# Kernel tuning notes

Measured on AMD Instinct MI355X. Metric: run time of the kernel, lower is better.

Reference implementation:

```python
import jax, jax.numpy as jnp
import numpy as np

NB, HD, NL, NF = 5, 64, 4, 10           # num_bins, hidden_dim(d_model), num_layers, num_frames
DI, DS, DC, DTR = 128, 16, 4, 4          # d_inner=2*HD, d_state, d_conv, dt_rank=ceil(HD/16)
B, H, W = 4, 64, 64


def _conv2d(x, w, b):
    y = jax.lax.conv_general_dilated(x, w, (1, 1), 'SAME',
                                     dimension_numbers=('NCHW', 'OIHW', 'NCHW'))
    return y + b[None, :, None, None]


def _bn_relu(x, gamma, beta, eps=1e-5):
    # BatchNorm2d in training mode: biased batch stats over (N,H,W)
    mean = x.mean(axis=(0, 2, 3), keepdims=True)
    var = x.var(axis=(0, 2, 3), keepdims=True)
    y = (x - mean) * jax.lax.rsqrt(var + eps)
    return jax.nn.relu(y * gamma[None, :, None, None] + beta[None, :, None, None])


def _silu(x):
    return x * jax.nn.sigmoid(x)


def _causal_dwconv(x, w, b):
    # x: (B,L,DI), w: (DI,K) depthwise causal conv, b: (DI,)
    K = w.shape[1]
    L = x.shape[1]
    xp = jnp.pad(x, ((0, 0), (K - 1, 0), (0, 0)))
    y = sum(xp[:, k:k + L, :] * w[:, k] for k in range(K))
    return y + b


def _selective_scan(u, delta, A, Bm, Cm, D):
    # u,delta: (B,L,DI); A: (DI,DS); Bm,Cm: (B,L,DS); D: (DI,)
    dT, BT, CT, uT = (t.transpose(1, 0, 2) for t in (delta, Bm, Cm, u))
    h0 = jnp.zeros((u.shape[0], A.shape[0], A.shape[1]), u.dtype)

    def step(h, inp):
        d_t, B_t, C_t, u_t = inp                     # (B,DI),(B,DS),(B,DS),(B,DI)
        dA = jnp.exp(d_t[:, :, None] * A)            # (B,DI,DS)
        h = dA * h + (d_t * u_t)[:, :, None] * B_t[:, None, :]
        y = jnp.einsum('bds,bs->bd', h, C_t)
        return h, y

    _, ys = jax.lax.scan(step, h0, (dT, BT, CT, uT))  # ys: (L,B,DI)
    return ys.transpose(1, 0, 2) + u * D


def _mamba(x, in_proj, conv_w, conv_b, x_proj, dt_w, dt_b, A_log, Dp, out_proj):
    xz = x @ in_proj.T                               # (B,L,2*DI)
    xi, z = jnp.split(xz, 2, axis=-1)
    xi = _silu(_causal_dwconv(xi, conv_w, conv_b))
    xdbc = xi @ x_proj.T                             # (B,L,DTR+2*DS)
    dt, Bm, Cm = jnp.split(xdbc, [DTR, DTR + DS], axis=-1)
    delta = jax.nn.softplus(dt @ dt_w.T + dt_b)
    A = -jnp.exp(A_log)
    y = _selective_scan(xi, delta, A, Bm, Cm, Dp)
    return (y * _silu(z)) @ out_proj.T


def setup_inputs() -> dict:
    key = jax.random.key(0)
    ks = jax.random.split(key, 20)
    s = 0.02
    inp = {
        'x': jax.random.normal(ks[0], (B, NB, H, W), jnp.float32),
        'enc_w': jax.random.normal(ks[1], (HD, NB, 3, 3), jnp.float32) * s,
        'enc_b': jnp.zeros((HD,), jnp.float32),
        'enc_g': jnp.ones((HD,), jnp.float32),
        'enc_be': jnp.zeros((HD,), jnp.float32),
        'in_proj': jax.random.normal(ks[2], (NL, 2 * DI, HD), jnp.float32) * s,
        'conv_w': jax.random.normal(ks[3], (NL, DI, DC), jnp.float32) * s,
        'conv_b': jnp.zeros((NL, DI), jnp.float32),
        'x_proj': jax.random.normal(ks[4], (NL, DTR + 2 * DS, DI), jnp.float32) * s,
        'dt_w': jax.random.normal(ks[5], (NL, DI, DTR), jnp.float32) * s,
        'dt_b': jax.random.normal(ks[6], (NL, DI), jnp.float32) * 0.1 - 4.0,
        'A_log': jnp.broadcast_to(jnp.log(jnp.arange(1, DS + 1, dtype=jnp.float32)),
                                  (NL, DI, DS)).copy(),
        'Dp': jnp.ones((NL, DI), jnp.float32),
        'out_proj': jax.random.normal(ks[7], (NL, HD, DI), jnp.float32) * s,
        'dec1_w': jax.random.normal(ks[8], (HD, HD, 3, 3), jnp.float32) * s,
        'dec1_b': jnp.zeros((HD,), jnp.float32),
        'dec1_g': jnp.ones((HD,), jnp.float32),
        'dec1_be': jnp.zeros((HD,), jnp.float32),
        'dec2_w': jax.random.normal(ks[9], (NF, HD, 3, 3), jnp.float32) * s,
        'dec2_b': jnp.zeros((NF,), jnp.float32),
    }
    return inp


def reference(x, enc_w, enc_b, enc_g, enc_be, in_proj, conv_w, conv_b, x_proj,
              dt_w, dt_b, A_log, Dp, out_proj, dec1_w, dec1_b, dec1_g, dec1_be,
              dec2_w, dec2_b):
    Bb, _, Hh, Ww = x.shape
    h = _bn_relu(_conv2d(x, enc_w, enc_b), enc_g, enc_be)   # (B,HD,H,W)
    t = h.reshape(Bb, HD, Hh * Ww).transpose(0, 2, 1)        # (B,L,HD)
    for i in range(NL):
        t = t + _mamba(t, in_proj[i], conv_w[i], conv_b[i], x_proj[i],
                       dt_w[i], dt_b[i], A_log[i], Dp[i], out_proj[i])
    h = t.transpose(0, 2, 1).reshape(Bb, HD, Hh, Ww)
    h = _bn_relu(_conv2d(h, dec1_w, dec1_b), dec1_g, dec1_be)
    return _conv2d(h, dec2_w, dec2_b)                        # (B,NF,H,W)
```

## Files before the change

### kernel.cpp

```cpp
#include <hip/hip_runtime.h>
#include <hip/hip_bf16.h>

#define BB   4
#define NBC  5
#define HD   64
#define NLAYER 4
#define NFC  10
#define DIM  128
#define DSN  16
#define DCN  4
#define DTRK 4
#define HH   64
#define WWD  64
#define LL   4096
#define MM   (BB*LL)
#define CLEN   32
#define NCHUNK 128

#define A4GET(a, i) (((i) & 3) == 0 ? (a)[(i) >> 2].x : ((i) & 3) == 1 ? (a)[(i) >> 2].y : \
                     ((i) & 3) == 2 ? (a)[(i) >> 2].z : (a)[(i) >> 2].w)

__global__ void k_prep_all(const float* __restrict__ in_proj, const float* __restrict__ out_proj,
                           const float* __restrict__ dec1_w, const float* __restrict__ dec2_w,
                           float* __restrict__ wTin, float* __restrict__ wTout,
                           float* __restrict__ wT1, float* __restrict__ wT2,
                           float* __restrict__ stats, float* __restrict__ stats2) {
    int idx = blockIdx.x * blockDim.x + threadIdx.x;
    if (idx < 65536) {
        int n = idx & 255, k = (idx >> 8) & 63, l = idx >> 14;
        wTin[idx] = in_proj[(l << 14) + (n << 6) + k];
    } else if (idx < 98304) {
        int j = idx - 65536;
        int n = j & 63, k = (j >> 6) & 127, l = j >> 13;
        wTout[j] = out_proj[(l << 13) + (n << 7) + k];
    } else if (idx < 135168) {
        int j = idx - 98304;
        int co = j & 63, tap = (j >> 6) % 9, ci = j / 576;
        wT1[j] = dec1_w[co * 576 + ci * 9 + tap];
    } else if (idx < 142848) {
        int j = idx - 135168;
        int tap = j % 12, t2 = j / 12, co = t2 % NFC, ci = t2 / NFC;
        wT2[j] = (tap < 9) ? dec2_w[co * 576 + ci * 9 + tap] : 0.f;
    } else if (idx < 143104) {
        int j = idx - 142848;
        if (j < 128) stats[j] = 0.f; else stats2[j - 128] = 0.f;
    }
}

__global__ void k_enc_conv(const float* __restrict__ x, const float* __restrict__ w,
                           const float* __restrict__ bias, float* __restrict__ out,
                           float* __restrict__ stats) {
    __shared__ float r1[256], r2[256];
    int tid = threadIdx.x;
    int idx = blockIdx.x * 256 + tid;
    int wx = idx & 63;
    int hy = (idx >> 6) & 63;
    int co = (idx >> 12) & 63;
    int b  = idx >> 18;
    float acc = bias[co];
    for (int ci = 0; ci < NBC; ++ci) {
        const float* xin = x + (((long)(b * NBC + ci)) << 12);
        const float* wp  = w + (co * NBC + ci) * 9;
        #pragma unroll
        for (int kh = 0; kh < 3; ++kh) {
            int ih = hy + kh - 1;
            if (ih < 0 || ih >= HH) continue;
            #pragma unroll
            for (int kw = 0; kw < 3; ++kw) {
                int iw = wx + kw - 1;
                if (iw < 0 || iw >= WWD) continue;
                acc += xin[(ih << 6) + iw] * wp[kh * 3 + kw];
            }
        }
    }
    out[idx] = acc;
    r1[tid] = acc; r2[tid] = acc * acc;
    __syncthreads();
    for (int off = 128; off > 0; off >>= 1) {
        if (tid < off) { r1[tid] += r1[tid + off]; r2[tid] += r2[tid + off]; }
        __syncthreads();
    }
    if (tid == 0) {
        atomicAdd(&stats[co], r1[0]);
        atomicAdd(&stats[64 + co], r2[0]);
    }
}

__global__ __launch_bounds__(256, 1) void k_gemm_in_bn(const float* __restrict__ src,
                                                       const float* __restrict__ stats,
                                                       const float* __restrict__ g,
                                                       const float* __restrict__ be,
                                                       const float* __restrict__ wT,
                                                       float* __restrict__ tout,
                                                       float* __restrict__ xz) {
    __shared__ __align__(16) float ts[64 * 68];
    __shared__ float sc[64], sh[64];
    long m0 = (long)blockIdx.x << 6;
    int b = (int)(m0 >> 12);
    int hw0 = (int)(m0 & 4095);
    int tid = threadIdx.x;
    if (tid < 64) {
        float m = stats[tid] * (1.f / 16384.f);
        float var = stats[64 + tid] * (1.f / 16384.f) - m * m;
        float ss = g[tid] * rsqrtf(var + 1e-5f);
        sc[tid] = ss; sh[tid] = be[tid] - m * ss;
    }
    __syncthreads();
    for (int i = tid; i < 4096; i += 256) {
        int pix = i & 63, c = i >> 6;
        float v = src[(((long)((b << 6) + c)) << 12) + hw0 + pix];
        ts[pix * 68 + c] = fmaxf(v * sc[c] + sh[c], 0.f);
    }
    __syncthreads();
    for (int i = tid; i < 4096; i += 256) {
        int r = i >> 6, c = i & 63;
        tout[(m0 + r) * 64 + c] = ts[r * 68 + c];
    }
    int rg = tid >> 5;
    int cg = tid & 31;
    float acc[8][8] = {};
    int n0 = cg << 3;
    for (int k4 = 0; k4 < 16; ++k4) {
        float4 a[8];
        #pragma unroll
        for (int r2 = 0; r2 < 8; ++r2)
            a[r2] = *(const float4*)&ts[((rg << 3) + r2) * 68 + (k4 << 2)];
        #pragma unroll
        for (int kk = 0; kk < 4; ++kk) {
            const float* wr = wT + (((k4 << 2) + kk) << 8) + n0;
            float4 w0 = *(const float4*)&wr[0];
            float4 w1 = *(const float4*)&wr[4];
            #pragma unroll
            for (int r2 = 0; r2 < 8; ++r2) {
                float av = (kk == 0) ? a[r2].x : (kk == 1) ? a[r2].y
                         : (kk == 2) ? a[r2].z : a[r2].w;
                acc[r2][0] += av * w0.x; acc[r2][1] += av * w0.y;
                acc[r2][2] += av * w0.z; acc[r2][3] += av * w0.w;
                acc[r2][4] += av * w1.x; acc[r2][5] += av * w1.y;
                acc[r2][6] += av * w1.z; acc[r2][7] += av * w1.w;
            }
        }
    }
    #pragma unroll
    for (int r2 = 0; r2 < 8; ++r2) {
        long m = m0 + (rg << 3) + r2;
        *(float4*)&xz[(m << 8) + n0]     = make_float4(acc[r2][0], acc[r2][1], acc[r2][2], acc[r2][3]);
        *(float4*)&xz[(m << 8) + n0 + 4] = make_float4(acc[r2][4], acc[r2][5], acc[r2][6], acc[r2][7]);
    }
}

__global__ __launch_bounds__(512, 4) void k_xproj_fused(
        const float* __restrict__ xz, const float* __restrict__ cw,
        const float* __restrict__ cb, const float* __restrict__ Wx,
        const float* __restrict__ dw, const float* __restrict__ dbias,
        const float* __restrict__ A_log,
        float* __restrict__ xiT, float* __restrict__ deltaT,
        float* __restrict__ xdbc, float* __restrict__ Pb, float* __restrict__ Sb) {
    __shared__ __align__(16) float xz_s[35 * 132];
    __shared__ __align__(16) float xi_s[32 * 132];
    __shared__ __align__(16) float w_s[36 * 132];
    __shared__ __align__(16) float xs[32 * 40];
    __shared__ float cwT[4 * 128];
    __shared__ float cb_s[128];
    long m0 = (long)blockIdx.x << 5;
    int l0 = (int)(m0 & 4095);
    int tid = threadIdx.x;

    for (int i = tid; i < 35 * 32; i += 512) {
        int j = i >> 5, c4 = (i & 31) << 2;
        float4 v = make_float4(0.f, 0.f, 0.f, 0.f);
        if (l0 - 3 + j >= 0) v = *(const float4*)&xz[(m0 - 3 + j) * 256 + c4];
        *(float4*)&xz_s[j * 132 + c4] = v;
    }
    if (tid < 128) cb_s[tid] = cb[tid];
    { int kk = tid >> 7, dii = tid & 127; if (tid < 512) cwT[(kk << 7) + dii] = cw[(dii << 2) + kk]; }
    for (int i = tid; i < 1152; i += 512) {
        int n = i >> 5, c4 = (i & 31) << 2;
        *(float4*)&w_s[n * 132 + c4] = *(const float4*)&Wx[(n << 7) + c4];
    }
    __syncthreads();

    #pragma unroll
    for (int ii = 0; ii < 2; ++ii) {
        int i = tid + (ii << 9);
        int r = i >> 5, d4 = (i & 31) << 2;
        float4 a = *(const float4*)&cb_s[d4];
        #pragma unroll
        for (int kk = 0; kk < 4; ++kk) {
            float4 xv = *(const float4*)&xz_s[(r + kk) * 132 + d4];
            float4 wv = *(const float4*)&cwT[(kk << 7) + d4];
            a.x += xv.x * wv.x; a.y += xv.y * wv.y;
            a.z += xv.z * wv.z; a.w += xv.w * wv.w;
        }
        a.x = a.x / (1.f + __expf(-a.x));
        a.y = a.y / (1.f + __expf(-a.y));
        a.z = a.z / (1.f + __expf(-a.z));
        a.w = a.w / (1.f + __expf(-a.w));
        *(float4*)&xi_s[r * 132 + d4] = a;
    }
    __syncthreads();

    {
        int n = tid & 63, rg6 = tid >> 6;
        if (n < 36) {
            float acc[4] = {0, 0, 0, 0};
            for (int k4 = 0; k4 < 32; ++k4) {
                float4 w4 = *(const float4*)&w_s[n * 132 + (k4 << 2)];
                #pragma unroll
                for (int r = 0; r < 4; ++r) {
                    float4 a4 = *(const float4*)&xi_s[((rg6 << 2) + r) * 132 + (k4 << 2)];
                    acc[r] += a4.x * w4.x + a4.y * w4.y + a4.z * w4.z + a4.w * w4.w;
                }
            }
            #pragma unroll
            for (int r = 0; r < 4; ++r) {
                int rr = (rg6 << 2) + r;
                xdbc[(m0 + rr) * 36 + n] = acc[r];
                xs[rr * 40 + n] = acc[r];
            }
        }
    }
    __syncthreads();

    float* delta_s = xz_s;
    for (int i = tid; i < 4096; i += 512) {
        int r = i >> 7, di2 = i & 127;
        float4 d4 = *(const float4*)&dw[di2 << 2];
        float v = dbias[di2]
                + xs[r * 40 + 0] * d4.x + xs[r * 40 + 1] * d4.y
                + xs[r * 40 + 2] * d4.z + xs[r * 40 + 3] * d4.w;
        float sp = (v > 20.f) ? v : log1pf(expf(v));
        delta_s[r * 132 + di2] = sp;
    }
    __syncthreads();

    {
        int dii = tid & 127, q = tid >> 7;
        float td[8], tu[8];
        #pragma unroll
        for (int j = 0; j < 8; ++j) {
            td[j] = delta_s[((q << 3) + j) * 132 + dii];
            tu[j] = xi_s[((q << 3) + j) * 132 + dii];
        }
        long tb = (long)dii * MM + m0 + (q << 3);
        *(float4*)&deltaT[tb]     = make_float4(td[0], td[1], td[2], td[3]);
        *(float4*)&deltaT[tb + 4] = make_float4(td[4], td[5], td[6], td[7]);
        *(float4*)&xiT[tb]        = make_float4(tu[0], tu[1], tu[2], tu[3]);
        *(float4*)&xiT[tb + 4]    = make_float4(tu[4], tu[5], tu[6], tu[7]);
    }

    {
        int di = tid >> 2;
        int dso = (tid & 3) << 2;
        float4 al = *(const float4*)&A_log[(di << 4) + dso];
        float Av[4] = { -expf(al.x), -expf(al.y), -expf(al.z), -expf(al.w) };
        float h[4] = {0, 0, 0, 0};
        float P[4] = {1, 1, 1, 1};
        #pragma unroll 4
        for (int i = 0; i < CLEN; ++i) {
            float d = delta_s[i * 132 + di];
            float u = xi_s[i * 132 + di];
            float du = d * u;
            float4 B0 = *(const float4*)&xs[i * 40 + DTRK + dso];
            float a0 = __expf(d * Av[0]); h[0] = a0 * h[0] + du * B0.x; P[0] *= a0;
            float a1 = __expf(d * Av[1]); h[1] = a1 * h[1] + du * B0.y; P[1] *= a1;
            float a2 = __expf(d * Av[2]); h[2] = a2 * h[2] + du * B0.z; P[2] *= a2;
            float a3 = __expf(d * Av[3]); h[3] = a3 * h[3] + du * B0.w; P[3] *= a3;
        }
        long o = ((long)blockIdx.x << 11) + (di << 4) + dso;
        *(float4*)&Pb[o] = make_float4(P[0], P[1], P[2], P[3]);
        *(float4*)&Sb[o] = make_float4(h[0], h[1], h[2], h[3]);
    }
}

__global__ void k_scan_p2(const float* __restrict__ Pb, float* Sb) {
    int t = blockIdx.x * blockDim.x + threadIdx.x;
    int b = t >> 11;
    int s = t & 2047;
    long base = (long)b << 18;
    float p[4], sv[4];
    #pragma unroll
    for (int k = 0; k < 4; ++k) {
        long idx = base + ((long)k << 11) + s;
        p[k] = Pb[idx]; sv[k] = Sb[idx];
    }
    float h = 0.f;
    for (int c = 0; c < 32; ++c) {
        float np[4] = {0, 0, 0, 0}, ns[4] = {0, 0, 0, 0};
        if (c < 31) {
            #pragma unroll
            for (int k = 0; k < 4; ++k) {
                long idx = base + ((long)(((c + 1) << 2) + k) << 11) + s;
                np[k] = Pb[idx]; ns[k] = Sb[idx];
            }
        }
        long i0 = base + ((long)(c << 2) << 11) + s;
        Sb[i0]        = h;  h = p[0] * h + sv[0];
        Sb[i0 + 2048] = h;  h = p[1] * h + sv[1];
        Sb[i0 + 4096] = h;  h = p[2] * h + sv[2];
        Sb[i0 + 6144] = h;  h = p[3] * h + sv[3];
        #pragma unroll
        for (int k = 0; k < 4; ++k) { p[k] = np[k]; sv[k] = ns[k]; }
    }
}

__global__ __launch_bounds__(256, 4) void k_scan_p3_oi(
        float* xz, const float* __restrict__ xiT, const float* __restrict__ deltaT,
        const float* __restrict__ xdbc,
        const float* __restrict__ A_log, const float* __restrict__ Dp,
        const float* __restrict__ wTo, const float* __restrict__ wTi,
        float* __restrict__ tio, const float* __restrict__ h0g, int doB) {
    __shared__ __align__(16) float u_s[CLEN * 132];
    __shared__ __align__(16) float bc_s[CLEN * 36];
    __shared__ __align__(16) float t_s[CLEN * 68];
    long m0 = (long)blockIdx.x << 5;
    int tid = threadIdx.x;
    int di = tid >> 1;
    int odd = tid & 1;
    int dso = odd << 3;

    const float* colp = (odd ? xiT : deltaT) + (long)di * MM + m0;
    float4 a4[8];
    #pragma unroll
    for (int j = 0; j < 8; ++j) a4[j] = *(const float4*)&colp[j << 2];

    #pragma unroll
    for (int ii = 0; ii < 4; ++ii) {
        int i = tid + (ii << 8);
        int r = i >> 5, c4 = (i & 31) << 2;
        *(float4*)&u_s[r * 132 + c4] = *(const float4*)&xz[((m0 + r) << 8) + DIM + c4];
    }
    for (int i = tid; i < CLEN * 9; i += 256) {
        int r = i / 9, c4 = (i - r * 9) << 2;
        *(float4*)&bc_s[r * 36 + c4] = *(const float4*)&xdbc[(m0 + r) * 36 + c4];
    }
    float4 al0 = *(const float4*)&A_log[(di << 4) + dso];
    float4 al1 = *(const float4*)&A_log[(di << 4) + dso + 4];
    float Av[8] = { -expf(al0.x), -expf(al0.y), -expf(al0.z), -expf(al0.w),
                    -expf(al1.x), -expf(al1.y), -expf(al1.z), -expf(al1.w) };
    float Dv = Dp[di];
    long o = ((long)blockIdx.x << 11) + (di << 4) + dso;
    float4 h04 = *(const float4*)&h0g[o];
    float4 h14 = *(const float4*)&h0g[o + 4];
    float h[8] = { h04.x, h04.y, h04.z, h04.w, h14.x, h14.y, h14.z, h14.w };
    __syncthreads();

    #pragma unroll
    for (int i = 0; i < CLEN; ++i) {
        float own = A4GET(a4, i);
        float oth = __shfl_xor(own, 1);
        float d = odd ? oth : own;
        float u = odd ? own : oth;
        float du = d * u;
        const float* bc = &bc_s[i * 36];
        float4 B0 = *(const float4*)&bc[DTRK + dso];
        float4 B1 = *(const float4*)&bc[DTRK + dso + 4];
        float4 C0 = *(const float4*)&bc[DTRK + DSN + dso];
        float4 C1 = *(const float4*)&bc[DTRK + DSN + dso + 4];
        float a0 = __expf(d * Av[0]); h[0] = a0 * h[0] + du * B0.x;
        float a1 = __expf(d * Av[1]); h[1] = a1 * h[1] + du * B0.y;
        float a2 = __expf(d * Av[2]); h[2] = a2 * h[2] + du * B0.z;
        float a3 = __expf(d * Av[3]); h[3] = a3 * h[3] + du * B0.w;
        float a4s = __expf(d * Av[4]); h[4] = a4s * h[4] + du * B1.x;
        float a5 = __expf(d * Av[5]); h[5] = a5 * h[5] + du * B1.y;
        float a6 = __expf(d * Av[6]); h[6] = a6 * h[6] + du * B1.z;
        float a7 = __expf(d * Av[7]); h[7] = a7 * h[7] + du * B1.w;
        float yp = h[0] * C0.x + h[1] * C0.y + h[2] * C0.z + h[3] * C0.w
                 + h[4] * C1.x + h[5] * C1.y + h[6] * C1.z + h[7] * C1.w;
        yp += __shfl_xor(yp, 1);
        if (!odd) {
            float z = u_s[i * 132 + di];
            u_s[i * 132 + di] = (yp + u * Dv) * (z / (1.f + __expf(-z)));
        }
    }
    __syncthreads();

    {
        int rg = tid >> 4, cg = tid & 15;
        int n0 = cg << 2;
        float acc[2][4] = {};
        for (int k4 = 0; k4 < 32; ++k4) {
            float4 a0 = *(const float4*)&u_s[(rg << 1) * 132 + (k4 << 2)];
            float4 a1 = *(const float4*)&u_s[((rg << 1) + 1) * 132 + (k4 << 2)];
            #pragma unroll
            for (int kk = 0; kk < 4; ++kk) {
                const float* wr = wTo + (((k4 << 2) + kk) << 6) + n0;
                float4 w0 = *(const float4*)&wr[0];
                float av0 = (kk == 0) ? a0.x : (kk == 1) ? a0.y : (kk == 2) ? a0.z : a0.w;
                float av1 = (kk == 0) ? a1.x : (kk == 1) ? a1.y : (kk == 2) ? a1.z : a1.w;
                acc[0][0] += av0 * w0.x; acc[0][1] += av0 * w0.y;
                acc[0][2] += av0 * w0.z; acc[0][3] += av0 * w0.w;
                acc[1][0] += av1 * w0.x; acc[1][1] += av1 * w0.y;
                acc[1][2] += av1 * w0.z; acc[1][3] += av1 * w0.w;
            }
        }
        #pragma unroll
        for (int r2 = 0; r2 < 2; ++r2) {
            long m = m0 + (rg << 1) + r2;
            float4 tv = *(const float4*)&tio[(m << 6) + n0];
            tv.x += acc[r2][0]; tv.y += acc[r2][1];
            tv.z += acc[r2][2]; tv.w += acc[r2][3];
            *(float4*)&tio[(m << 6) + n0] = tv;
            *(float4*)&t_s[((rg << 1) + r2) * 68 + n0] = tv;
        }
    }
    if (!doB) return;
    __syncthreads();

    {
        int rg = tid >> 5, cgn = tid & 31;
        int n0 = cgn << 3;
        float acc[4][8] = {};
        for (int k4 = 0; k4 < 16; ++k4) {
            float4 a[4];
            #pragma unroll
            for (int r2 = 0; r2 < 4; ++r2)
                a[r2] = *(const float4*)&t_s[((rg << 2) + r2) * 68 + (k4 << 2)];
            #pragma unroll
            for (int kk = 0; kk < 4; ++kk) {
                const float* wr = wTi + (((k4 << 2) + kk) << 8) + n0;
                float4 w0 = *(const float4*)&wr[0];
                float4 w1 = *(const float4*)&wr[4];
                #pragma unroll
                for (int r2 = 0; r2 < 4; ++r2) {
                    float av = (kk == 0) ? a[r2].x : (kk == 1) ? a[r2].y
                             : (kk == 2) ? a[r2].z : a[r2].w;
                    acc[r2][0] += av * w0.x; acc[r2][1] += av * w0.y;
                    acc[r2][2] += av * w0.z; acc[r2][3] += av * w0.w;
                    acc[r2][4] += av * w1.x; acc[r2][5] += av * w1.y;
                    acc[r2][6] += av * w1.z; acc[r2][7] += av * w1.w;
                }
            }
        }
        #pragma unroll
        for (int r2 = 0; r2 < 4; ++r2) {
            long m = m0 + (rg << 2) + r2;
            *(float4*)&xz[(m << 8) + n0]     = make_float4(acc[r2][0], acc[r2][1], acc[r2][2], acc[r2][3]);
            *(float4*)&xz[(m << 8) + n0 + 4] = make_float4(acc[r2][4], acc[r2][5], acc[r2][6], acc[r2][7]);
        }
    }
}

__global__ __launch_bounds__(256, 1) void k_dec1_new(const float* __restrict__ tin,
                                                     const float* __restrict__ wT,
                                                     const float* __restrict__ bias,
                                                     float* __restrict__ out,
                                                     float* __restrict__ stats2) {
    __shared__ __align__(16) float x_s[64 * 132];
    __shared__ __align__(16) float w_s[4 * 4608];
    int tile = blockIdx.x;
    int b = blockIdx.y;
    int ty0 = (tile >> 3) << 3;
    int tx0 = (tile & 7) << 3;
    int tid = threadIdx.x;
    int wv = tid >> 6;
    int lane = tid & 63;
    int r = lane >> 3;
    int cg = lane & 7;

    for (int i = tid; i < 6400; i += 256) {
        int pl = i >> 6;
        int c = i & 63;
        int py = pl / 10, px = pl - py * 10;
        int ih = ty0 + py - 1, iw = tx0 + px - 1;
        float v = 0.f;
        if (ih >= 0 && ih < HH && iw >= 0 && iw < WWD)
            v = tin[(((long)((b << 12) + (ih << 6) + iw)) << 6) + c];
        x_s[c * 132 + py * 12 + px] = v;
    }
    float* myw = &w_s[wv * 4608];
    const float* gw = wT + (wv * 16) * 576;
    float4 pref[18];
    #pragma unroll
    for (int i = 0; i < 18; ++i)
        pref[i] = *(const float4*)&gw[(i * 64 + lane) * 4];
    #pragma unroll
    for (int i = 0; i < 18; ++i)
        *(float4*)&myw[(i * 64 + lane) * 4] = pref[i];
    __syncthreads();

    float acc[8][8] = {};
    #pragma unroll
    for (int ch = 0; ch < 2; ++ch) {
        if (ch == 0) {
            const float* gw1 = wT + (wv * 16 + 8) * 576;
            #pragma unroll
            for (int i = 0; i < 18; ++i)
                pref[i] = *(const float4*)&gw1[(i * 64 + lane) * 4];
        }
        for (int cl = 0; cl < 8; ++cl) {
            int cib = wv * 16 + ch * 8 + cl;
            float xrow[3][10];
            #pragma unroll
            for (int kh = 0; kh < 3; ++kh) {
                const float* xr = &x_s[cib * 132 + (r + kh) * 12];
                float4 a0 = *(const float4*)&xr[0];
                float4 a1 = *(const float4*)&xr[4];
                float2 a2 = *(const float2*)&xr[8];
                xrow[kh][0] = a0.x; xrow[kh][1] = a0.y; xrow[kh][2] = a0.z; xrow[kh][3] = a0.w;
                xrow[kh][4] = a1.x; xrow[kh][5] = a1.y; xrow[kh][6] = a1.z; xrow[kh][7] = a1.w;
                xrow[kh][8] = a2.x; xrow[kh][9] = a2.y;
            }
            const float* wp = &myw[cl * 576];
            #pragma unroll
            for (int kh = 0; kh < 3; ++kh) {
                #pragma unroll
                for (int kw = 0; kw < 3; ++kw) {
                    const float* wp2 = wp + (kh * 3 + kw) * 64 + (cg << 3);
                    float4 wa = *(const float4*)&wp2[0];
                    float4 wb = *(const float4*)&wp2[4];
                    #pragma unroll
                    for (int j = 0; j < 8; ++j) {
                        float xv = xrow[kh][kw + j];
                        acc[j][0] += xv * wa.x; acc[j][1] += xv * wa.y;
                        acc[j][2] += xv * wa.z; acc[j][3] += xv * wa.w;
                        acc[j][4] += xv * wb.x; acc[j][5] += xv * wb.y;
                        acc[j][6] += xv * wb.z; acc[j][7] += xv * wb.w;
                    }
                }
            }
        }
        if (ch == 0) {
            #pragma unroll
            for (int i = 0; i < 18; ++i)
                *(float4*)&myw[(i * 64 + lane) * 4] = pref[i];
        }
    }

    #pragma unroll
    for (int j = 0; j < 8; ++j) {
        *(float4*)&myw[lane * 68 + (j << 3)]     = make_float4(acc[j][0], acc[j][1], acc[j][2], acc[j][3]);
        *(float4*)&myw[lane * 68 + (j << 3) + 4] = make_float4(acc[j][4], acc[j][5], acc[j][6], acc[j][7]);
    }
    __syncthreads();

    float bv = bias[lane];
    float ssum = 0.f, ssq = 0.f;
    #pragma unroll
    for (int pp = 0; pp < 16; ++pp) {
        int pr = (wv << 1) + (pp >> 3);
        int pc = pp & 7;
        int ol = (pr << 3) + (lane >> 3);
        int ix = (pc << 3) + (lane & 7);
        float s = w_s[ol * 68 + ix] + w_s[4608 + ol * 68 + ix]
                + w_s[9216 + ol * 68 + ix] + w_s[13824 + ol * 68 + ix] + bv;
        out[(((long)((b << 12) + ((ty0 + pr) << 6) + tx0 + pc)) << 6) + lane] = s;
        ssum += s; ssq += s * s;
    }
    float* red = x_s;
    red[(wv << 6) + lane] = ssum;
    red[256 + (wv << 6) + lane] = ssq;
    __syncthreads();
    if (tid < 64) {
        float a = red[tid] + red[64 + tid] + red[128 + tid] + red[192 + tid];
        float q = red[256 + tid] + red[320 + tid] + red[384 + tid] + red[448 + tid];
        atomicAdd(&stats2[tid], a);
        atomicAdd(&stats2[64 + tid], q);
    }
}

__global__ void k_dec2_fused(const float* __restrict__ src, const float* __restrict__ stats2,
                             const float* __restrict__ g, const float* __restrict__ be,
                             const float* __restrict__ wT, const float* __restrict__ bias,
                             float* __restrict__ out) {
    __shared__ float x_s[64 * 101];
    __shared__ float w_s[64 * NFC * 12];
    __shared__ float sc_s[64];
    __shared__ float sh_s[64];
    int tile = blockIdx.x;
    int b = blockIdx.y;
    int ty0 = (tile >> 3) << 3;
    int tx0 = (tile & 7) << 3;
    int tid = threadIdx.x;

    if (tid < 64) {
        float m = stats2[tid] * (1.f / 16384.f);
        float var = stats2[64 + tid] * (1.f / 16384.f) - m * m;
        float s = g[tid] * rsqrtf(var + 1e-5f);
        sc_s[tid] = s;
        sh_s[tid] = be[tid] - m * s;
    }
    for (int i = tid; i < 64 * NFC * 12; i += 256)
        w_s[i] = wT[i];
    __syncthreads();

    for (int i = tid; i < 6400; i += 256) {
        int pl = i >> 6;
        int c = i & 63;
        int py = pl / 10, px = pl - py * 10;
        int ih = ty0 + py - 1, iw = tx0 + px - 1;
        float v = 0.f;
        if (ih >= 0 && ih < HH && iw >= 0 && iw < WWD) {
            v = src[((long)((b << 12) + (ih << 6) + iw)) * 64 + c];
            v = fmaxf(v * sc_s[c] + sh_s[c], 0.f);
        }
        x_s[c * 101 + pl] = v;
    }
    __syncthreads();

    int px = tid & 63;
    int py = px >> 3, pxx = px & 7;
    int cog = tid >> 6;
    float acc[3] = {0.f, 0.f, 0.f};
    int nco = (cog < 2) ? 3 : 2;

    for (int ci = 0; ci < 64; ++ci) {
        const float* xr = &x_s[ci * 101 + py * 10 + pxx];
        float xv[9];
        #pragma unroll
        for (int kh = 0; kh < 3; ++kh)
            #pragma unroll
            for (int kw = 0; kw < 3; ++kw)
                xv[kh * 3 + kw] = xr[kh * 10 + kw];
        #pragma unroll
        for (int j = 0; j < 3; ++j) {
            if (j >= nco) break;
            int co = cog + (j << 2);
            const float* wp = &w_s[(ci * NFC + co) * 12];
            float4 w0 = *(const float4*)&wp[0];
            float4 w1 = *(const float4*)&wp[4];
            float  w8 = wp[8];
            acc[j] += xv[0] * w0.x + xv[1] * w0.y + xv[2] * w0.z + xv[3] * w0.w
                    + xv[4] * w1.x + xv[5] * w1.y + xv[6] * w1.z + xv[7] * w1.w
                    + xv[8] * w8;
        }
    }
    int hw = ((ty0 + py) << 6) + tx0 + pxx;
    #pragma unroll
    for (int j = 0; j < 3; ++j) {
        if (j >= nco) break;
        int co = cog + (j << 2);
        out[((long)(b * NFC + co) << 12) + hw] = acc[j] + bias[co];
    }
}

extern "C" void kernel_launch(void* const* d_in, const int* in_sizes, int n_in,
                              void* d_out, int out_size, void* d_ws, size_t ws_size,
                              hipStream_t stream) {
    const float* x       = (const float*)d_in[0];
    const float* enc_w   = (const float*)d_in[1];
    const float* enc_b   = (const float*)d_in[2];
    const float* enc_g   = (const float*)d_in[3];
    const float* enc_be  = (const float*)d_in[4];
    const float* in_proj = (const float*)d_in[5];
    const float* conv_w  = (const float*)d_in[6];
    const float* conv_b  = (const float*)d_in[7];
    const float* x_proj  = (const float*)d_in[8];
    const float* dt_w    = (const float*)d_in[9];
    const float* dt_b    = (const float*)d_in[10];
    const float* A_log   = (const float*)d_in[11];
    const float* Dp      = (const float*)d_in[12];
    const float* out_prj = (const float*)d_in[13];
    const float* dec1_w  = (const float*)d_in[14];
    const float* dec1_b  = (const float*)d_in[15];
    const float* dec1_g  = (const float*)d_in[16];
    const float* dec1_be = (const float*)d_in[17];
    const float* dec2_w  = (const float*)d_in[18];
    const float* dec2_b  = (const float*)d_in[19];
    float* out = (float*)d_out;

    float* ws = (float*)d_ws;
    size_t off = 0;
    float* conv_buf  = ws + off; off += 1048576;
    float* stats     = ws + off; off += 128;
    float* stats2    = ws + off; off += 128;
    float* wT1       = ws + off; off += 36864;
    float* wT2       = ws + off; off += 7680;
    float* wTin      = ws + off; off += 65536;
    float* wTout     = ws + off; off += 32768;
    float* t_buf     = ws + off; off += 1048576;
    float* xz_buf    = ws + off; off += 4194304;
    float* xiT_buf   = ws + off; off += 2097152;
    float* deltaT_buf= ws + off; off += 2097152;
    float* xdbc_buf  = ws + off; off += 589824;
    float* Pb        = ws + off; off += 1048576;
    float* Sb        = ws + off; off += 1048576;
    (void)ws_size; (void)in_sizes; (void)n_in; (void)out_size;

    k_prep_all<<<560, 256, 0, stream>>>(in_proj, out_prj, dec1_w, dec2_w,
                                        wTin, wTout, wT1, wT2, stats, stats2);

    k_enc_conv<<<4096, 256, 0, stream>>>(x, enc_w, enc_b, conv_buf, stats);

    k_gemm_in_bn<<<256, 256, 0, stream>>>(conv_buf, stats, enc_g, enc_be, wTin,
                                          t_buf, xz_buf);

    for (int i = 0; i < NLAYER; ++i) {
        int doB = (i < NLAYER - 1) ? 1 : 0;
        k_xproj_fused<<<512, 512, 0, stream>>>(
            xz_buf, conv_w + i * DIM * DCN, conv_b + i * DIM, x_proj + i * 36 * DIM,
            dt_w + i * DIM * DTRK, dt_b + i * DIM, A_log + i * DIM * DSN,
            xiT_buf, deltaT_buf, xdbc_buf, Pb, Sb);
        k_scan_p2<<<32, 256, 0, stream>>>(Pb, Sb);
        k_scan_p3_oi<<<512, 256, 0, stream>>>(
            xz_buf, xiT_buf, deltaT_buf, xdbc_buf,
            A_log + i * DIM * DSN, Dp + i * DIM,
            wTout + i * 8192, wTin + ((i + 1) & 3) * 16384,
            t_buf, Sb, doB);
    }

    dim3 dg1(64, BB);
    k_dec1_new<<<dg1, 256, 0, stream>>>(t_buf, wT1, dec1_b, conv_buf, stats2);
    k_dec2_fused<<<dg1, 256, 0, stream>>>(conv_buf, stats2, dec1_g, dec1_be, wT2, dec2_b, out);
}
```

Baseline: 502.4 us.

## Fuse all Mamba layers into one persistent kernel with software grid barriers

Replaces the per-layer trio of kernels (xproj/chunk-scan, inter-chunk prefix, scan+out/in projection) with a single persistent 512-block kernel that loops over layers and synchronises with an atomic grid barrier. Each block keeps its delta, xi and B/C values in shared memory across the phases, so the transposed xiT/deltaT/xdbc global buffers and their round trips go away, along with 11 kernel launches. The price is three grid barriers per layer, a serialized inter-chunk phase on only 16 blocks while the others spin, and reliance on all 512 blocks being co-resident; the barrier gives up after a spin limit instead of deadlocking, which could silently break correctness.

Result: slower. 1.932 ms (+284.5%).

```diff
diff --git a/kernel.cpp b/kernel.cpp
--- a/kernel.cpp
+++ b/kernel.cpp
@@ -16,15 +16,14 @@
 #define MM   (BB*LL)
 #define CLEN   32
 #define NCHUNK 128
-
-#define A4GET(a, i) (((i) & 3) == 0 ? (a)[(i) >> 2].x : ((i) & 3) == 1 ? (a)[(i) >> 2].y : \
-                     ((i) & 3) == 2 ? (a)[(i) >> 2].z : (a)[(i) >> 2].w)
+#define NBLK   512
 
 __global__ void k_prep_all(const float* __restrict__ in_proj, const float* __restrict__ out_proj,
                            const float* __restrict__ dec1_w, const float* __restrict__ dec2_w,
                            float* __restrict__ wTin, float* __restrict__ wTout,
                            float* __restrict__ wT1, float* __restrict__ wT2,
-                           float* __restrict__ stats, float* __restrict__ stats2) {
+                           float* __restrict__ stats, float* __restrict__ stats2,
+                           float* __restrict__ barF) {
     int idx = blockIdx.x * blockDim.x + threadIdx.x;
     if (idx < 65536) {
         int n = idx & 255, k = (idx >> 8) & 63, l = idx >> 14;
@@ -44,7 +43,30 @@
     } else if (idx < 143104) {
         int j = idx - 142848;
         if (j < 128) stats[j] = 0.f; else stats2[j - 128] = 0.f;
-    }
+    } else if (idx < 143112) {
+        barF[idx - 143104] = 0.f;
+    }
+}
+
+__device__ __forceinline__ void grid_barrier(int* bar) {
+    __syncthreads();
+    if (threadIdx.x == 0) {
+        __threadfence();
+        int g = __hip_atomic_load(&bar[1], __ATOMIC_RELAXED, __HIP_MEMORY_SCOPE_AGENT);
+        int prev = __hip_atomic_fetch_add(&bar[0], 1, __ATOMIC_ACQ_REL, __HIP_MEMORY_SCOPE_AGENT);
+        if (prev == NBLK - 1) {
+            __hip_atomic_store(&bar[0], 0, __ATOMIC_RELAXED, __HIP_MEMORY_SCOPE_AGENT);
+            __hip_atomic_store(&bar[1], g + 1, __ATOMIC_RELEASE, __HIP_MEMORY_SCOPE_AGENT);
+        } else {
+            int spins = 0;
+            while (__hip_atomic_load(&bar[1], __ATOMIC_ACQUIRE, __HIP_MEMORY_SCOPE_AGENT) == g) {
+                __builtin_amdgcn_s_sleep(8);
+                if (++spins > (1 << 20)) break;
+            }
+        }
+        __threadfence();
+    }
+    __syncthreads();
 }
 
 __global__ void k_enc_conv(const float* __restrict__ x, const float* __restrict__ w,
@@ -149,295 +171,246 @@
     }
 }
 
-__global__ __launch_bounds__(512, 4) void k_xproj_fused(
-        const float* __restrict__ xz, const float* __restrict__ cw,
-        const float* __restrict__ cb, const float* __restrict__ Wx,
-        const float* __restrict__ dw, const float* __restrict__ dbias,
-        const float* __restrict__ A_log,
-        float* __restrict__ xiT, float* __restrict__ deltaT,
-        float* __restrict__ xdbc, float* __restrict__ Pb, float* __restrict__ Sb) {
+__global__ __launch_bounds__(512, 4) void k_mamba_mega(
+        float* xz, const float* __restrict__ cw_all, const float* __restrict__ cb_all,
+        const float* __restrict__ Wx_all, const float* __restrict__ dw_all,
+        const float* __restrict__ db_all, const float* __restrict__ Al_all,
+        const float* __restrict__ Dp_all, const float* __restrict__ wTo_all,
+        const float* __restrict__ wTi_all, float* __restrict__ tio,
+        float* __restrict__ Pb, float* __restrict__ Sb, int* bar) {
     __shared__ __align__(16) float xz_s[35 * 132];
     __shared__ __align__(16) float xi_s[32 * 132];
-    __shared__ __align__(16) float w_s[36 * 132];
     __shared__ __align__(16) float xs[32 * 40];
+    __shared__ __align__(16) float t_s[32 * 68];
     __shared__ float cwT[4 * 128];
     __shared__ float cb_s[128];
-    long m0 = (long)blockIdx.x << 5;
+
+    int tid = threadIdx.x;
+    int bid = blockIdx.x;
+    long m0 = (long)bid << 5;
     int l0 = (int)(m0 & 4095);
-    int tid = threadIdx.x;
-
-    for (int i = tid; i < 35 * 32; i += 512) {
-        int j = i >> 5, c4 = (i & 31) << 2;
-        float4 v = make_float4(0.f, 0.f, 0.f, 0.f);
-        if (l0 - 3 + j >= 0) v = *(const float4*)&xz[(m0 - 3 + j) * 256 + c4];
-        *(float4*)&xz_s[j * 132 + c4] = v;
-    }
-    if (tid < 128) cb_s[tid] = cb[tid];
-    { int kk = tid >> 7, dii = tid & 127; if (tid < 512) cwT[(kk << 7) + dii] = cw[(dii << 2) + kk]; }
-    for (int i = tid; i < 1152; i += 512) {
-        int n = i >> 5, c4 = (i & 31) << 2;
-        *(float4*)&w_s[n * 132 + c4] = *(const float4*)&Wx[(n << 7) + c4];
-    }
-    __syncthreads();
-
-    #pragma unroll
-    for (int ii = 0; ii < 2; ++ii) {
-        int i = tid + (ii << 9);
-        int r = i >> 5, d4 = (i & 31) << 2;
-        float4 a = *(const float4*)&cb_s[d4];
+
+    for (int il = 0; il < NLAYER; ++il) {
+        const float* cw    = cw_all + il * DIM * DCN;
+        const float* cb    = cb_all + il * DIM;
+        const float* Wx    = Wx_all + il * 36 * DIM;
+        const float* dw    = dw_all + il * DIM * DTRK;
+        const float* dbias = db_all + il * DIM;
+        const float* A_log = Al_all + il * DIM * DSN;
+        const float* Dp    = Dp_all + il * DIM;
+        const float* wTo   = wTo_all + il * 8192;
+        const float* wTi   = wTi_all + (((il + 1) & 3) * 16384);
+
+        for (int i = tid; i < 35 * 32; i += 512) {
+            int j = i >> 5, c4 = (i & 31) << 2;
+            float4 v = make_float4(0.f, 0.f, 0.f, 0.f);
+            if (l0 - 3 + j >= 0) v = *(const float4*)&xz[(m0 - 3 + j) * 256 + c4];
+            *(float4*)&xz_s[j * 132 + c4] = v;
+        }
+        if (tid < 128) cb_s[tid] = cb[tid];
+        { int kk = tid >> 7, dii = tid & 127; cwT[(kk << 7) + dii] = cw[(dii << 2) + kk]; }
+        __syncthreads();
+
         #pragma unroll
-        for (int kk = 0; kk < 4; ++kk) {
-            float4 xv = *(const float4*)&xz_s[(r + kk) * 132 + d4];
-            float4 wv = *(const float4*)&cwT[(kk << 7) + d4];
-            a.x += xv.x * wv.x; a.y += xv.y * wv.y;
-            a.z += xv.z * wv.z; a.w += xv.w * wv.w;
-        }
-        a.x = a.x / (1.f + __expf(-a.x));
-        a.y = a.y / (1.f + __expf(-a.y));
-        a.z = a.z / (1.f + __expf(-a.z));
-        a.w = a.w / (1.f + __expf(-a.w));
-        *(float4*)&xi_s[r * 132 + d4] = a;
-    }
-    __syncthreads();
-
-    {
-        int n = tid & 63, rg6 = tid >> 6;
-        if (n < 36) {
-            float acc[4] = {0, 0, 0, 0};
+        for (int ii = 0; ii < 2; ++ii) {
+            int i = tid + (ii << 9);
+            int r = i >> 5, d4 = (i & 31) << 2;
+            float4 a = *(const float4*)&cb_s[d4];
+            #pragma unroll
+            for (int kk = 0; kk < 4; ++kk) {
+                float4 xv = *(const float4*)&xz_s[(r + kk) * 132 + d4];
+                float4 wv = *(const float4*)&cwT[(kk << 7) + d4];
+                a.x += xv.x * wv.x; a.y += xv.y * wv.y;
+                a.z += xv.z * wv.z; a.w += xv.w * wv.w;
+            }
+            a.x = a.x / (1.f + __expf(-a.x));
+            a.y = a.y / (1.f + __expf(-a.y));
+            a.z = a.z / (1.f + __expf(-a.z));
+            a.w = a.w / (1.f + __expf(-a.w));
+            *(float4*)&xi_s[r * 132 + d4] = a;
+        }
+        __syncthreads();
+
+        {
+            int n = tid & 63, rg6 = tid >> 6;
+            if (n < 36) {
+                float acc[4] = {0, 0, 0, 0};
+                for (int k4 = 0; k4 < 32; ++k4) {
+                    float4 w4 = *(const float4*)&Wx[(n << 7) + (k4 << 2)];
+                    #pragma unroll
+                    for (int r = 0; r < 4; ++r) {
+                        float4 a4 = *(const float4*)&xi_s[((rg6 << 2) + r) * 132 + (k4 << 2)];
+                        acc[r] += a4.x * w4.x + a4.y * w4.y + a4.z * w4.z + a4.w * w4.w;
+                    }
+                }
+                #pragma unroll
+                for (int r = 0; r < 4; ++r)
+                    xs[((rg6 << 2) + r) * 40 + n] = acc[r];
+            }
+        }
+        __syncthreads();
+
+        float* delta_s = xz_s;
+        for (int i = tid; i < 4096; i += 512) {
+            int r = i >> 7, di2 = i & 127;
+            float4 d4 = *(const float4*)&dw[di2 << 2];
+            float v = dbias[di2]
+                    + xs[r * 40 + 0] * d4.x + xs[r * 40 + 1] * d4.y
+                    + xs[r * 40 + 2] * d4.z + xs[r * 40 + 3] * d4.w;
+            float sp = (v > 20.f) ? v : log1pf(expf(v));
+            delta_s[r * 132 + di2] = sp;
+        }
+        __syncthreads();
+
+        {
+            int di = tid >> 2;
+            int dso = (tid & 3) << 2;
+            float4 al = *(const float4*)&A_log[(di << 4) + dso];
+            float Av[4] = { -expf(al.x), -expf(al.y), -expf(al.z), -expf(al.w) };
+            float h[4] = {0, 0, 0, 0};
+            float P[4] = {1, 1, 1, 1};
+            #pragma unroll 4
+            for (int i = 0; i < CLEN; ++i) {
+                float d = delta_s[i * 132 + di];
+                float u = xi_s[i * 132 + di];
+                float du = d * u;
+                float4 B0 = *(const float4*)&xs[i * 40 + DTRK + dso];
+                float a0 = __expf(d * Av[0]); h[0] = a0 * h[0] + du * B0.x; P[0] *= a0;
+                float a1 = __expf(d * Av[1]); h[1] = a1 * h[1] + du * B0.y; P[1] *= a1;
+                float a2 = __expf(d * Av[2]); h[2] = a2 * h[2] + du * B0.z; P[2] *= a2;
+                float a3 = __expf(d * Av[3]); h[3] = a3 * h[3] + du * B0.w; P[3] *= a3;
+            }
+            long o = ((long)bid << 11) + (di << 4) + dso;
+            *(float4*)&Pb[o] = make_float4(P[0], P[1], P[2], P[3]);
+            *(float4*)&Sb[o] = make_float4(h[0], h[1], h[2], h[3]);
+        }
+        grid_barrier(bar);
+
+        if (bid < 16) {
+            int t = (bid << 9) | tid;
+            int b = t >> 11;
+            int s = t & 2047;
+            long base = (long)b << 18;
+            float p[4], sv[4];
+            #pragma unroll
+            for (int k = 0; k < 4; ++k) {
+                long idx = base + ((long)k << 11) + s;
+                p[k] = Pb[idx]; sv[k] = Sb[idx];
+            }
+            float h = 0.f;
+            for (int c = 0; c < 32; ++c) {
+                float np[4] = {0, 0, 0, 0}, ns[4] = {0, 0, 0, 0};
+                if (c < 31) {
+                    #pragma unroll
+                    for (int k = 0; k < 4; ++k) {
+                        long idx = base + ((long)(((c + 1) << 2) + k) << 11) + s;
+                        np[k] = Pb[idx]; ns[k] = Sb[idx];
+                    }
+                }
+                long i0 = base + ((long)(c << 2) << 11) + s;
+                Sb[i0]        = h;  h = p[0] * h + sv[0];
+                Sb[i0 + 2048] = h;  h = p[1] * h + sv[1];
+                Sb[i0 + 4096] = h;  h = p[2] * h + sv[2];
+                Sb[i0 + 6144] = h;  h = p[3] * h + sv[3];
+                #pragma unroll
+                for (int k = 0; k < 4; ++k) { p[k] = np[k]; sv[k] = ns[k]; }
+            }
+        }
+        grid_barrier(bar);
+
+        {
+            int di = tid >> 2;
+            int dsel = tid & 3;
+            int dso = dsel << 2;
+            float zq[8];
+            #pragma unroll
+            for (int j = 0; j < 8; ++j)
+                zq[j] = xz[(m0 + (dsel << 3) + j) * 256 + DIM + di];
+            float4 al = *(const float4*)&A_log[(di << 4) + dso];
+            float Av[4] = { -expf(al.x), -expf(al.y), -expf(al.z), -expf(al.w) };
+            float Dv = Dp[di];
+            long o = ((long)bid << 11) + (di << 4) + dso;
+            float4 h04 = *(const float4*)&Sb[o];
+            float h[4] = { h04.x, h04.y, h04.z, h04.w };
+            #pragma unroll
+            for (int i = 0; i < CLEN; ++i) {
+                float d = delta_s[i * 132 + di];
+                float u = xi_s[i * 132 + di];
+                float du = d * u;
+                float4 B0 = *(const float4*)&xs[i * 40 + DTRK + dso];
+                float4 C0 = *(const float4*)&xs[i * 40 + DTRK + DSN + dso];
+                float a0 = __expf(d * Av[0]); h[0] = a0 * h[0] + du * B0.x;
+                float a1 = __expf(d * Av[1]); h[1] = a1 * h[1] + du * B0.y;
+                float a2 = __expf(d * Av[2]); h[2] = a2 * h[2] + du * B0.z;
+                float a3 = __expf(d * Av[3]); h[3] = a3 * h[3] + du * B0.w;
+                float yp = h[0] * C0.x + h[1] * C0.y + h[2] * C0.z + h[3] * C0.w;
+                yp += __shfl_xor(yp, 1);
+                yp += __shfl_xor(yp, 2);
+                if (dsel == (i >> 3)) {
+                    float z = zq[i & 7];
+                    xi_s[i * 132 + di] = (yp + u * Dv) * (z / (1.f + __expf(-z)));
+                }
+            }
+        }
+        __syncthreads();
+
+        {
+            int rg = tid >> 4, cg = tid & 15;
+            int n0 = cg << 2;
+            float acc4[4] = {};
             for (int k4 = 0; k4 < 32; ++k4) {
-                float4 w4 = *(const float4*)&w_s[n * 132 + (k4 << 2)];
+                float4 a0 = *(const float4*)&xi_s[rg * 132 + (k4 << 2)];
                 #pragma unroll
-                for (int r = 0; r < 4; ++r) {
-                    float4 a4 = *(const float4*)&xi_s[((rg6 << 2) + r) * 132 + (k4 << 2)];
-                    acc[r] += a4.x * w4.x + a4.y * w4.y + a4.z * w4.z + a4.w * w4.w;
+                for (int kk = 0; kk < 4; ++kk) {
+                    const float* wr = wTo + (((k4 << 2) + kk) << 6) + n0;
+                    float4 w0 = *(const float4*)&wr[0];
+                    float av = (kk == 0) ? a0.x : (kk == 1) ? a0.y : (kk == 2) ? a0.z : a0.w;
+                    acc4[0] += av * w0.x; acc4[1] += av * w0.y;
+                    acc4[2] += av * w0.z; acc4[3] += av * w0.w;
                 }
             }
-            #pragma unroll
-            for (int r = 0; r < 4; ++r) {
-                int rr = (rg6 << 2) + r;
-                xdbc[(m0 + rr) * 36 + n] = acc[r];
-                xs[rr * 40 + n] = acc[r];
-            }
-        }
-    }
-    __syncthreads();
-
-    float* delta_s = xz_s;
-    for (int i = tid; i < 4096; i += 512) {
-        int r = i >> 7, di2 = i & 127;
-        float4 d4 = *(const float4*)&dw[di2 << 2];
-        float v = dbias[di2]
-                + xs[r * 40 + 0] * d4.x + xs[r * 40 + 1] * d4.y
-                + xs[r * 40 + 2] * d4.z + xs[r * 40 + 3] * d4.w;
-        float sp = (v > 20.f) ? v : log1pf(expf(v));
-        delta_s[r * 132 + di2] = sp;
-    }
-    __syncthreads();
-
-    {
-        int dii = tid & 127, q = tid >> 7;
-        float td[8], tu[8];
-        #pragma unroll
-        for (int j = 0; j < 8; ++j) {
-            td[j] = delta_s[((q << 3) + j) * 132 + dii];
-            tu[j] = xi_s[((q << 3) + j) * 132 + dii];
-        }
-        long tb = (long)dii * MM + m0 + (q << 3);
-        *(float4*)&deltaT[tb]     = make_float4(td[0], td[1], td[2], td[3]);
-        *(float4*)&deltaT[tb + 4] = make_float4(td[4], td[5], td[6], td[7]);
-        *(float4*)&xiT[tb]        = make_float4(tu[0], tu[1], tu[2], tu[3]);
-        *(float4*)&xiT[tb + 4]    = make_float4(tu[4], tu[5], tu[6], tu[7]);
-    }
-
-    {
-        int di = tid >> 2;
-        int dso = (tid & 3) << 2;
-        float4 al = *(const float4*)&A_log[(di << 4) + dso];
-        float Av[4] = { -expf(al.x), -expf(al.y), -expf(al.z), -expf(al.w) };
-        float h[4] = {0, 0, 0, 0};
-        float P[4] = {1, 1, 1, 1};
-        #pragma unroll 4
-        for (int i = 0; i < CLEN; ++i) {
-            float d = delta_s[i * 132 + di];
-            float u = xi_s[i * 132 + di];
-            float du = d * u;
-            float4 B0 = *(const float4*)&xs[i * 40 + DTRK + dso];
-            float a0 = __expf(d * Av[0]); h[0] = a0 * h[0] + du * B0.x; P[0] *= a0;
-            float a1 = __expf(d * Av[1]); h[1] = a1 * h[1] + du * B0.y; P[1] *= a1;
-            float a2 = __expf(d * Av[2]); h[2] = a2 * h[2] + du * B0.z; P[2] *= a2;
-            float a3 = __expf(d * Av[3]); h[3] = a3 * h[3] + du * B0.w; P[3] *= a3;
-        }
-        long o = ((long)blockIdx.x << 11) + (di << 4) + dso;
-        *(float4*)&Pb[o] = make_float4(P[0], P[1], P[2], P[3]);
-        *(float4*)&Sb[o] = make_float4(h[0], h[1], h[2], h[3]);
-    }
-}
-
-__global__ void k_scan_p2(const float* __restrict__ Pb, float* Sb) {
-    int t = blockIdx.x * blockDim.x + threadIdx.x;
-    int b = t >> 11;
-    int s = t & 2047;
-    long base = (long)b << 18;
-    float p[4], sv[4];
-    #pragma unroll
-    for (int k = 0; k < 4; ++k) {
-        long idx = base + ((long)k << 11) + s;
-        p[k] = Pb[idx]; sv[k] = Sb[idx];
-    }
-    float h = 0.f;
-    for (int c = 0; c < 32; ++c) {
-        float np[4] = {0, 0, 0, 0}, ns[4] = {0, 0, 0, 0};
-        if (c < 31) {
-            #pragma unroll
-            for (int k = 0; k < 4; ++k) {
-                long idx = base + ((long)(((c + 1) << 2) + k) << 11) + s;
-                np[k] = Pb[idx]; ns[k] = Sb[idx];
-            }
-        }
-        long i0 = base + ((long)(c << 2) << 11) + s;
-        Sb[i0]        = h;  h = p[0] * h + sv[0];
-        Sb[i0 + 2048] = h;  h = p[1] * h + sv[1];
-        Sb[i0 + 4096] = h;  h = p[2] * h + sv[2];
-        Sb[i0 + 6144] = h;  h = p[3] * h + sv[3];
-        #pragma unroll
-        for (int k = 0; k < 4; ++k) { p[k] = np[k]; sv[k] = ns[k]; }
-    }
-}
-
-__global__ __launch_bounds__(256, 4) void k_scan_p3_oi(
-        float* xz, const float* __restrict__ xiT, const float* __restrict__ deltaT,
-        const float* __restrict__ xdbc,
-        const float* __restrict__ A_log, const float* __restrict__ Dp,
-        const float* __restrict__ wTo, const float* __restrict__ wTi,
-        float* __restrict__ tio, const float* __restrict__ h0g, int doB) {
-    __shared__ __align__(16) float u_s[CLEN * 132];
-    __shared__ __align__(16) float bc_s[CLEN * 36];
-    __shared__ __align__(16) float t_s[CLEN * 68];
-    long m0 = (long)blockIdx.x << 5;
-    int tid = threadIdx.x;
-    int di = tid >> 1;
-    int odd = tid & 1;
-    int dso = odd << 3;
-
-    const float* colp = (odd ? xiT : deltaT) + (long)di * MM + m0;
-    float4 a4[8];
-    #pragma unroll
-    for (int j = 0; j < 8; ++j) a4[j] = *(const float4*)&colp[j << 2];
-
-    #pragma unroll
-    for (int ii = 0; ii < 4; ++ii) {
-        int i = tid + (ii << 8);
-        int r = i >> 5, c4 = (i & 31) << 2;
-        *(float4*)&u_s[r * 132 + c4] = *(const float4*)&xz[((m0 + r) << 8) + DIM + c4];
-    }
-    for (int i = tid; i < CLEN * 9; i += 256) {
-        int r = i / 9, c4 = (i - r * 9) << 2;
-        *(float4*)&bc_s[r * 36 + c4] = *(const float4*)&xdbc[(m0 + r) * 36 + c4];
-    }
-    float4 al0 = *(const float4*)&A_log[(di << 4) + dso];
-    float4 al1 = *(const float4*)&A_log[(di << 4) + dso + 4];
-    float Av[8] = { -expf(al0.x), -expf(al0.y), -expf(al0.z), -expf(al0.w),
-                    -expf(al1.x), -expf(al1.y), -expf(al1.z), -expf(al1.w) };
-    float Dv = Dp[di];
-    long o = ((long)blockIdx.x << 11) + (di << 4) + dso;
-    float4 h04 = *(const float4*)&h0g[o];
-    float4 h14 = *(const float4*)&h0g[o + 4];
-    float h[8] = { h04.x, h04.y, h04.z, h04.w, h14.x, h14.y, h14.z, h14.w };
-    __syncthreads();
-
-    #pragma unroll
-    for (int i = 0; i < CLEN; ++i) {
-        float own = A4GET(a4, i);
-        float oth = __shfl_xor(own, 1);
-        float d = odd ? oth : own;
-        float u = odd ? own : oth;
-        float du = d * u;
-        const float* bc = &bc_s[i * 36];
-        float4 B0 = *(const float4*)&bc[DTRK + dso];
-        float4 B1 = *(const float4*)&bc[DTRK + dso + 4];
-        float4 C0 = *(const float4*)&bc[DTRK + DSN + dso];
-        float4 C1 = *(const float4*)&bc[DTRK + DSN + dso + 4];
-        float a0 = __expf(d * Av[0]); h[0] = a0 * h[0] + du * B0.x;
-        float a1 = __expf(d * Av[1]); h[1] = a1 * h[1] + du * B0.y;
-        float a2 = __expf(d * Av[2]); h[2] = a2 * h[2] + du * B0.z;
-        float a3 = __expf(d * Av[3]); h[3] = a3 * h[3] + du * B0.w;
-        float a4s = __expf(d * Av[4]); h[4] = a4s * h[4] + du * B1.x;
-        float a5 = __expf(d * Av[5]); h[5] = a5 * h[5] + du * B1.y;
-        float a6 = __expf(d * Av[6]); h[6] = a6 * h[6] + du * B1.z;
-        float a7 = __expf(d * Av[7]); h[7] = a7 * h[7] + du * B1.w;
-        float yp = h[0] * C0.x + h[1] * C0.y + h[2] * C0.z + h[3] * C0.w
-                 + h[4] * C1.x + h[5] * C1.y + h[6] * C1.z + h[7] * C1.w;
-        yp += __shfl_xor(yp, 1);
-        if (!odd) {
-            float z = u_s[i * 132 + di];
-            u_s[i * 132 + di] = (yp + u * Dv) * (z / (1.f + __expf(-z)));
-        }
-    }
-    __syncthreads();
-
-    {
-        int rg = tid >> 4, cg = tid & 15;
-        int n0 = cg << 2;
-        float acc[2][4] = {};
-        for (int k4 = 0; k4 < 32; ++k4) {
-            float4 a0 = *(const float4*)&u_s[(rg << 1) * 132 + (k4 << 2)];
-            float4 a1 = *(const float4*)&u_s[((rg << 1) + 1) * 132 + (k4 << 2)];
-            #pragma unroll
-            for (int kk = 0; kk < 4; ++kk) {
-                const float* wr = wTo + (((k4 << 2) + kk) << 6) + n0;
-                float4 w0 = *(const float4*)&wr[0];
-                float av0 = (kk == 0) ? a0.x : (kk == 1) ? a0.y : (kk == 2) ? a0.z : a0.w;
-                float av1 = (kk == 0) ? a1.x : (kk == 1) ? a1.y : (kk == 2) ? a1.z : a1.w;
-                acc[0][0] += av0 * w0.x; acc[0][1] += av0 * w0.y;
-                acc[0][2] += av0 * w0.z; acc[0][3] += av0 * w0.w;
-                acc[1][0] += av1 * w0.x; acc[1][1] += av1 * w0.y;
-                acc[1][2] += av1 * w0.z; acc[1][3] += av1 * w0.w;
-            }
-        }
-        #pragma unroll
-        for (int r2 = 0; r2 < 2; ++r2) {
-            long m = m0 + (rg << 1) + r2;
+            long m = m0 + rg;
             float4 tv = *(const float4*)&tio[(m << 6) + n0];
-            tv.x += acc[r2][0]; tv.y += acc[r2][1];
-            tv.z += acc[r2][2]; tv.w += acc[r2][3];
+            tv.x += acc4[0]; tv.y += acc4[1];
+            tv.z += acc4[2]; tv.w += acc4[3];
             *(float4*)&tio[(m << 6) + n0] = tv;
-            *(float4*)&t_s[((rg << 1) + r2) * 68 + n0] = tv;
-        }
-    }
-    if (!doB) return;
-    __syncthreads();
-
-    {
-        int rg = tid >> 5, cgn = tid & 31;
-        int n0 = cgn << 3;
-        float acc[4][8] = {};
-        for (int k4 = 0; k4 < 16; ++k4) {
-            float4 a[4];
-            #pragma unroll
-            for (int r2 = 0; r2 < 4; ++r2)
-                a[r2] = *(const float4*)&t_s[((rg << 2) + r2) * 68 + (k4 << 2)];
-            #pragma unroll
-            for (int kk = 0; kk < 4; ++kk) {
-                const float* wr = wTi + (((k4 << 2) + kk) << 8) + n0;
-                float4 w0 = *(const float4*)&wr[0];
-                float4 w1 = *(const float4*)&wr[4];
+            *(float4*)&t_s[rg * 68 + n0] = tv;
+        }
+        if (il == NLAYER - 1) break;
+        __syncthreads();
+
+        {
+            int rg = tid >> 5, cgn = tid & 31;
+            int n0 = cgn << 3;
+            float acc[2][8] = {};
+            for (int k4 = 0; k4 < 16; ++k4) {
+                float4 a[2];
+                a[0] = *(const float4*)&t_s[(rg << 1) * 68 + (k4 << 2)];
+                a[1] = *(const float4*)&t_s[((rg << 1) + 1) * 68 + (k4 << 2)];
                 #pragma unroll
-                for (int r2 = 0; r2 < 4; ++r2) {
-                    float av = (kk == 0) ? a[r2].x : (kk == 1) ? a[r2].y
-                             : (kk == 2) ? a[r2].z : a[r2].w;
-                    acc[r2][0] += av * w0.x; acc[r2][1] += av * w0.y;
-                    acc[r2][2] += av * w0.z; acc[r2][3] += av * w0.w;
-                    acc[r2][4] += av * w1.x; acc[r2][5] += av * w1.y;
-                    acc[r2][6] += av * w1.z; acc[r2][7] += av * w1.w;
+                for (int kk = 0; kk < 4; ++kk) {
+                    const float* wr = wTi + (((k4 << 2) + kk) << 8) + n0;
+                    float4 w0 = *(const float4*)&wr[0];
+                    float4 w1 = *(const float4*)&wr[4];
+                    #pragma unroll
+                    for (int r2 = 0; r2 < 2; ++r2) {
+                        float av = (kk == 0) ? a[r2].x : (kk == 1) ? a[r2].y
+                                 : (kk == 2) ? a[r2].z : a[r2].w;
+                        acc[r2][0] += av * w0.x; acc[r2][1] += av * w0.y;
+                        acc[r2][2] += av * w0.z; acc[r2][3] += av * w0.w;
+                        acc[r2][4] += av * w1.x; acc[r2][5] += av * w1.y;
+                        acc[r2][6] += av * w1.z; acc[r2][7] += av * w1.w;
+                    }
                 }
             }
-        }
-        #pragma unroll
-        for (int r2 = 0; r2 < 4; ++r2) {
-            long m = m0 + (rg << 2) + r2;
-            *(float4*)&xz[(m << 8) + n0]     = make_float4(acc[r2][0], acc[r2][1], acc[r2][2], acc[r2][3]);
-            *(float4*)&xz[(m << 8) + n0 + 4] = make_float4(acc[r2][4], acc[r2][5], acc[r2][6], acc[r2][7]);
-        }
+            #pragma unroll
+            for (int r2 = 0; r2 < 2; ++r2) {
+                long m = m0 + (rg << 1) + r2;
+                *(float4*)&xz[(m << 8) + n0]     = make_float4(acc[r2][0], acc[r2][1], acc[r2][2], acc[r2][3]);
+                *(float4*)&xz[(m << 8) + n0 + 4] = make_float4(acc[r2][4], acc[r2][5], acc[r2][6], acc[r2][7]);
+            }
+        }
+        grid_barrier(bar);
     }
 }
 
@@ -670,34 +643,24 @@
     float* wTout     = ws + off; off += 32768;
     float* t_buf     = ws + off; off += 1048576;
     float* xz_buf    = ws + off; off += 4194304;
-    float* xiT_buf   = ws + off; off += 2097152;
-    float* deltaT_buf= ws + off; off += 2097152;
-    float* xdbc_buf  = ws + off; off += 589824;
     float* Pb        = ws + off; off += 1048576;
     float* Sb        = ws + off; off += 1048576;
+    float* barF      = ws + off; off += 8;
     (void)ws_size; (void)in_sizes; (void)n_in; (void)out_size;
 
+    int* bar = (int*)barF;
+
     k_prep_all<<<560, 256, 0, stream>>>(in_proj, out_prj, dec1_w, dec2_w,
-                                        wTin, wTout, wT1, wT2, stats, stats2);
+                                        wTin, wTout, wT1, wT2, stats, stats2, barF);
 
     k_enc_conv<<<4096, 256, 0, stream>>>(x, enc_w, enc_b, conv_buf, stats);
 
     k_gemm_in_bn<<<256, 256, 0, stream>>>(conv_buf, stats, enc_g, enc_be, wTin,
                                           t_buf, xz_buf);
 
-    for (int i = 0; i < NLAYER; ++i) {
-        int doB = (i < NLAYER - 1) ? 1 : 0;
-        k_xproj_fused<<<512, 512, 0, stream>>>(
-            xz_buf, conv_w + i * DIM * DCN, conv_b + i * DIM, x_proj + i * 36 * DIM,
-            dt_w + i * DIM * DTRK, dt_b + i * DIM, A_log + i * DIM * DSN,
-            xiT_buf, deltaT_buf, xdbc_buf, Pb, Sb);
-        k_scan_p2<<<32, 256, 0, stream>>>(Pb, Sb);
-        k_scan_p3_oi<<<512, 256, 0, stream>>>(
-            xz_buf, xiT_buf, deltaT_buf, xdbc_buf,
-            A_log + i * DIM * DSN, Dp + i * DIM,
-            wTout + i * 8192, wTin + ((i + 1) & 3) * 16384,
-            t_buf, Sb, doB);
-    }
+    k_mamba_mega<<<NBLK, 512, 0, stream>>>(
+        xz_buf, conv_w, conv_b, x_proj, dt_w, dt_b, A_log, Dp,
+        wTout, wTin, t_buf, Pb, Sb, bar);
 
     dim3 dg1(64, BB);
     k_dec1_new<<<dg1, 256, 0, stream>>>(t_buf, wT1, dec1_b, conv_buf, stats2);
```
